# Kernel tuning notes

Hardware: AMD Instinct MI355X
Metric: run time of the kernel (lower is better)

The kernel has to match this reference:

```python
import jax, jax.numpy as jnp
import numpy as np

N = 50000
E = 800000
IN_C = 512
HID = 256
OUT_C = 2
NUM_LAYERS = 3
NUM_HIER = 3
EPS = 1e-5


def setup_inputs() -> dict:
    key = jax.random.key(0)
    ks = jax.random.split(key, 24)
    g = lambda k, shp, fan: jax.random.normal(k, shp, jnp.float32) / np.sqrt(fan)
    inp = {
        "x": jax.random.normal(ks[0], (N, IN_C), jnp.float32),
        "edge_index": jax.random.randint(ks[1], (2, E), 0, N, jnp.int64),
        # GCN conv weights/biases
        "conv_w0": g(ks[2], (IN_C, HID), IN_C),
        "conv_ws": g(ks[3], (NUM_LAYERS - 1, HID, HID), HID),
        "conv_b": jnp.zeros((NUM_LAYERS, HID), jnp.float32),
        "bn_g": jnp.ones((NUM_LAYERS, HID), jnp.float32),
        "bn_b": jnp.zeros((NUM_LAYERS, HID), jnp.float32),
        # global-path MLPs
        "fcg_w0": g(ks[4], (HID, HID), HID),
        "fcg_ws": g(ks[5], (NUM_HIER - 1, 2 * HID, HID), 2 * HID),
        "fcg_b": jnp.zeros((NUM_HIER, HID), jnp.float32),
        "bng_g": jnp.ones((NUM_HIER, HID), jnp.float32),
        "bng_b": jnp.zeros((NUM_HIER, HID), jnp.float32),
        # local-path MLPs
        "fcl_w": g(ks[6], (NUM_HIER, HID, HID), HID),
        "fcl_b": jnp.zeros((NUM_HIER, HID), jnp.float32),
        "bnl_g": jnp.ones((NUM_HIER, HID), jnp.float32),
        "bnl_b": jnp.zeros((NUM_HIER, HID), jnp.float32),
        # output heads
        "outg_w": g(ks[7], (HID, OUT_C), HID),
        "outg_b": jnp.zeros((OUT_C,), jnp.float32),
        "outl_w": g(ks[8], (NUM_HIER, HID, OUT_C), HID),
        "outl_b": jnp.zeros((NUM_HIER, OUT_C), jnp.float32),
    }
    return inp


def _gcn_edges(edge_index):
    # add self-loops, compute symmetric normalization D^-1/2 (A+I) D^-1/2
    loops = jnp.arange(N, dtype=edge_index.dtype)
    rows = jnp.concatenate([edge_index[0], loops])
    cols = jnp.concatenate([edge_index[1], loops])
    deg = jax.ops.segment_sum(jnp.ones_like(rows, jnp.float32), rows, num_segments=N)
    dinv = jnp.where(deg > 0, jax.lax.rsqrt(deg), 0.0)
    w = dinv[rows] * dinv[cols]
    return rows, cols, w


def _propagate(h, rows, cols, w):
    msg = h[cols] * w[:, None]          # [E+N, HID] gather
    return jax.ops.segment_sum(msg, rows, num_segments=N)


def _bn(h, gamma, beta):
    m = h.mean(0)
    v = h.var(0)
    return gamma * (h - m) * jax.lax.rsqrt(v + EPS) + beta


def reference(x, edge_index, conv_w0, conv_ws, conv_b, bn_g, bn_b,
              fcg_w0, fcg_ws, fcg_b, bng_g, bng_b,
              fcl_w, fcl_b, bnl_g, bnl_b,
              outg_w, outg_b, outl_w, outl_b):
    rows, cols, ew = _gcn_edges(edge_index)
    h = x
    for i in range(NUM_LAYERS):
        W = conv_w0 if i == 0 else conv_ws[i - 1]
        h = _propagate(h @ W, rows, cols, ew) + conv_b[i]
        h = jax.nn.relu(_bn(h, bn_g[i], bn_b[i]))  # dropout = identity (eval)
    # hierarchical global path
    hg = []
    xg = jax.nn.relu(_bn(h @ fcg_w0 + fcg_b[0], bng_g[0], bng_b[0]))
    hg.append(xg)
    for i in range(NUM_HIER - 1):
        xg = jnp.concatenate([hg[i], h], -1) @ fcg_ws[i] + fcg_b[i + 1]
        xg = jax.nn.relu(_bn(xg, bng_g[i + 1], bng_b[i + 1]))
        hg.append(xg)
    og = jax.nn.log_softmax(hg[-1] @ outg_w + outg_b, axis=-1)
    # local heads
    ol = []
    for i in range(NUM_HIER):
        hl = jax.nn.relu(_bn(hg[i] @ fcl_w[i] + fcl_b[i], bnl_g[i], bnl_b[i]))
        ol.append(jax.nn.log_softmax(hl @ outl_w[i] + outl_b[i], axis=-1))
    # stack: [1 + NUM_HIER, N, OUT_C] (og first, then local heads)
    return jnp.stack([og] + ol, axis=0)
```

## Files before the change

kernel.cpp:

```cpp
#include <hip/hip_runtime.h>
#include <math.h>

#define N_NODES 50000
#define E_EDGES 800000
#define HID 256
#define EPS_BN 1e-5f

typedef __attribute__((ext_vector_type(8))) short short8;
typedef __attribute__((ext_vector_type(4))) float floatx4;
typedef __attribute__((ext_vector_type(8))) unsigned short ushort8v;

__device__ __forceinline__ unsigned short f2bf(float f) {
    unsigned u = __float_as_uint(f);
    u = (u + 0x7FFFu + ((u >> 16) & 1u)) >> 16;
    return (unsigned short)u;
}
__device__ __forceinline__ float bf2f(unsigned short b) {
    return __uint_as_float(((unsigned)b) << 16);
}
__device__ __forceinline__ void bn_scsh(const float* stats, const float* gamma,
                                        const float* beta, int ch,
                                        float& sc, float& sh) {
    const float invn = 1.0f / (float)N_NODES;
    float mean = stats[ch] * invn;
    float var = stats[HID + ch] * invn - mean * mean;
    var = fmaxf(var, 0.f);
    sc = gamma[ch] * rsqrtf(var + EPS_BN);
    sh = beta[ch] - mean * sc;
}

__global__ __launch_bounds__(256) void k_deg(const int* __restrict__ rows,
                                             int* __restrict__ deg) {
    int e = blockIdx.x * 256 + threadIdx.x;
    atomicAdd(&deg[rows[e]], 1);
}

__global__ __launch_bounds__(256) void k_dinv(const int* __restrict__ deg,
                                              float* __restrict__ dinv) {
    int n = blockIdx.x * 256 + threadIdx.x;
    if (n < N_NODES) dinv[n] = rsqrtf((float)deg[n] + 1.0f);
}

__global__ __launch_bounds__(1024) void k_scan(const int* __restrict__ deg,
                                               int* __restrict__ rowptr) {
    __shared__ int wsum[16];
    __shared__ int carry_s;
    int tid = threadIdx.x, lane = tid & 63, w = tid >> 6;
    if (tid == 0) carry_s = 0;
    __syncthreads();
    for (int base = 0; base < N_NODES; base += 1024) {
        int v = (base + tid < N_NODES) ? deg[base + tid] : 0;
        int x = v;
#pragma unroll
        for (int d = 1; d < 64; d <<= 1) {
            int t = __shfl_up(x, d);
            if (lane >= d) x += t;
        }
        if (lane == 63) wsum[w] = x;
        __syncthreads();
        if (w == 0) {
            int ws = (lane < 16) ? wsum[lane] : 0;
#pragma unroll
            for (int d = 1; d < 16; d <<= 1) {
                int t = __shfl_up(ws, d);
                if (lane >= d) ws += t;
            }
            if (lane < 16) wsum[lane] = ws;
        }
        __syncthreads();
        int c = carry_s;
        int wbase = (w > 0) ? wsum[w - 1] : 0;
        if (base + tid < N_NODES) rowptr[base + tid] = c + wbase + x - v;
        __syncthreads();
        if (tid == 0) carry_s = c + wsum[15];
        __syncthreads();
    }
    if (threadIdx.x == 0) rowptr[N_NODES] = carry_s;
}

__global__ __launch_bounds__(256) void k_fill(const int* __restrict__ rows,
                                              const int* __restrict__ cols,
                                              const int* __restrict__ rowptr,
                                              int* __restrict__ cursor,
                                              int* __restrict__ colidx) {
    int e = blockIdx.x * 256 + threadIdx.x;
    int r = rows[e];
    int pos = atomicAdd(&cursor[r], 1);
    colidx[rowptr[r] + pos] = cols[e];
}

__global__ __launch_bounds__(256) void k_f2bf_vec(const float* __restrict__ X,
                                                  unsigned short* __restrict__ Y,
                                                  int n4) {
    int i = blockIdx.x * 256 + threadIdx.x;
    if (i >= n4) return;
    float4 v = ((const float4*)X)[i];
    ushort4 o;
    o.x = f2bf(v.x); o.y = f2bf(v.y); o.z = f2bf(v.z); o.w = f2bf(v.w);
    ((ushort4*)Y)[i] = o;
}

__global__ __launch_bounds__(256) void k_wt(const float* __restrict__ W,
                                            unsigned short* __restrict__ Wt,
                                            int K) {
    int idx = blockIdx.x * 256 + threadIdx.x;
    if (idx >= K * HID) return;
    int k = idx >> 8;
    int n = idx & (HID - 1);
    Wt[(size_t)n * K + k] = f2bf(W[idx]);
}

__global__ __launch_bounds__(256) void k_gemm_mfma(
    const unsigned short* __restrict__ A0, int lda0,
    const unsigned short* __restrict__ A1, int lda1, int K0, int K,
    const unsigned short* __restrict__ Bt,
    unsigned short* __restrict__ C,
    const float* __restrict__ rowscale,
    float* __restrict__ stats)
{
    __shared__ alignas(16) unsigned short As[128 * 32];
    __shared__ alignas(16) unsigned short Bs[128 * 32];
    int tid = threadIdx.x;
    int wid = tid >> 6, lane = tid & 63;
    int row0 = blockIdx.x * 128;
    int n0 = blockIdx.y * 128;
    int wrow = (wid & 1) * 64, wcol = (wid >> 1) * 64;
    int lr = lane >> 2;
    int lk = (lane & 3) * 8;
    int qq = lane >> 4, mr = lane & 15;

    floatx4 acc[4][4];
#pragma unroll
    for (int i = 0; i < 4; ++i)
#pragma unroll
        for (int j = 0; j < 4; ++j) {
            floatx4 z = {0.f, 0.f, 0.f, 0.f};
            acc[i][j] = z;
        }

    for (int k0 = 0; k0 < K; k0 += 32) {
        const unsigned short* Abase;
        int lda;
        if (k0 < K0) { Abase = A0 + k0; lda = lda0; }
        else         { Abase = A1 + (k0 - K0); lda = lda1; }
#pragma unroll
        for (int i = 0; i < 2; ++i) {
            int rloc = wid * 32 + i * 16 + lr;
            int grow = row0 + rloc;
            if (grow > N_NODES - 1) grow = N_NODES - 1;
            const unsigned short* g = Abase + (size_t)grow * lda + lk;
            unsigned short* l = As + (wid * 32 + i * 16) * 32;
            __builtin_amdgcn_global_load_lds(
                (const __attribute__((address_space(1))) void*)g,
                (__attribute__((address_space(3))) void*)l, 16, 0, 0);
        }
#pragma unroll
        for (int i = 0; i < 2; ++i) {
            int nloc = wid * 32 + i * 16 + lr;
            const unsigned short* g = Bt + (size_t)(n0 + nloc) * K + k0 + lk;
            unsigned short* l = Bs + (wid * 32 + i * 16) * 32;
            __builtin_amdgcn_global_load_lds(
                (const __attribute__((address_space(1))) void*)g,
                (__attribute__((address_space(3))) void*)l, 16, 0, 0);
        }
        __syncthreads();
        short8 af[4], bfv[4];
#pragma unroll
        for (int i = 0; i < 4; ++i)
            af[i] = *(const short8*)(As + (wrow + i * 16 + mr) * 32 + qq * 8);
#pragma unroll
        for (int j = 0; j < 4; ++j)
            bfv[j] = *(const short8*)(Bs + (wcol + j * 16 + mr) * 32 + qq * 8);
#pragma unroll
        for (int i = 0; i < 4; ++i)
#pragma unroll
            for (int j = 0; j < 4; ++j)
                acc[i][j] = __builtin_amdgcn_mfma_f32_16x16x32_bf16(
                    af[i], bfv[j], acc[i][j], 0, 0, 0);
        __syncthreads();
    }

    float* ls = (float*)As;
    float* lq = ((float*)As) + 128;
    if (stats) {
        ((float*)As)[tid] = 0.f;
        __syncthreads();
    }

    float psum[4] = {0.f, 0.f, 0.f, 0.f};
    float psq[4]  = {0.f, 0.f, 0.f, 0.f};
#pragma unroll
    for (int i = 0; i < 4; ++i) {
        int rbase = row0 + wrow + i * 16 + qq * 4;
#pragma unroll
        for (int r = 0; r < 4; ++r) {
            int row = rbase + r;
            if (row >= N_NODES) continue;
            float rs = rowscale ? rowscale[row] : 1.0f;
            unsigned short* cp = C + (size_t)row * HID + n0 + wcol + mr;
#pragma unroll
            for (int j = 0; j < 4; ++j) {
                float v = acc[i][j][r] * rs;
                cp[j * 16] = f2bf(v);
                psum[j] += v;
                psq[j] += v * v;
            }
        }
    }
    if (stats) {
#pragma unroll
        for (int j = 0; j < 4; ++j) {
            int lc = wcol + j * 16 + mr;
            atomicAdd(&ls[lc], psum[j]);
            atomicAdd(&lq[lc], psq[j]);
        }
        __syncthreads();
        if (tid < 128) atomicAdd(&stats[n0 + tid], ls[tid]);
        else atomicAdd(&stats[HID + n0 + (tid - 128)], lq[tid - 128]);
    }
}

__global__ __launch_bounds__(256) void k_aggregate_bf(
    const unsigned short* __restrict__ g,
    unsigned short* __restrict__ outp,
    const int* __restrict__ rowptr,
    const int* __restrict__ colidx,
    const float* __restrict__ dinv,
    float* __restrict__ stats) {
    int lane = threadIdx.x & 63;
    int gw = blockIdx.x * 4 + (threadIdx.x >> 6);
    int totw = gridDim.x * 4;
    float s0 = 0.f, s1 = 0.f, s2 = 0.f, s3 = 0.f;
    float q0 = 0.f, q1 = 0.f, q2 = 0.f, q3 = 0.f;
    for (int node = gw; node < N_NODES; node += totw) {
        int s = rowptr[node], e = rowptr[node + 1];
        ushort4 sv = ((const ushort4*)(g + (size_t)node * HID))[lane];
        float a0 = bf2f(sv.x), a1 = bf2f(sv.y), a2 = bf2f(sv.z), a3 = bf2f(sv.w);
        for (int base = s; base < e; base += 64) {
            int cnt = e - base; if (cnt > 64) cnt = 64;
            int cidx = (lane < cnt) ? colidx[base + lane] : 0;
            int j = 0;
            for (; j + 4 <= cnt; j += 4) {
                int c0 = __shfl(cidx, j + 0), c1 = __shfl(cidx, j + 1);
                int c2 = __shfl(cidx, j + 2), c3 = __shfl(cidx, j + 3);
                ushort4 v0 = ((const ushort4*)(g + (size_t)c0 * HID))[lane];
                ushort4 v1 = ((const ushort4*)(g + (size_t)c1 * HID))[lane];
                ushort4 v2 = ((const ushort4*)(g + (size_t)c2 * HID))[lane];
                ushort4 v3 = ((const ushort4*)(g + (size_t)c3 * HID))[lane];
                a0 += (bf2f(v0.x) + bf2f(v1.x)) + (bf2f(v2.x) + bf2f(v3.x));
                a1 += (bf2f(v0.y) + bf2f(v1.y)) + (bf2f(v2.y) + bf2f(v3.y));
                a2 += (bf2f(v0.z) + bf2f(v1.z)) + (bf2f(v2.z) + bf2f(v3.z));
                a3 += (bf2f(v0.w) + bf2f(v1.w)) + (bf2f(v2.w) + bf2f(v3.w));
            }
            for (; j < cnt; ++j) {
                int c = __shfl(cidx, j);
                ushort4 v = ((const ushort4*)(g + (size_t)c * HID))[lane];
                a0 += bf2f(v.x); a1 += bf2f(v.y); a2 += bf2f(v.z); a3 += bf2f(v.w);
            }
        }
        float rs = dinv[node];
        a0 *= rs; a1 *= rs; a2 *= rs; a3 *= rs;
        ushort4 o;
        o.x = f2bf(a0); o.y = f2bf(a1); o.z = f2bf(a2); o.w = f2bf(a3);
        ((ushort4*)(outp + (size_t)node * HID))[lane] = o;
        s0 += a0; s1 += a1; s2 += a2; s3 += a3;
        q0 += a0 * a0; q1 += a1 * a1; q2 += a2 * a2; q3 += a3 * a3;
    }
    __shared__ float ls[HID], lq[HID];
    ls[threadIdx.x] = 0.f; lq[threadIdx.x] = 0.f;
    __syncthreads();
    atomicAdd(&ls[lane * 4 + 0], s0); atomicAdd(&lq[lane * 4 + 0], q0);
    atomicAdd(&ls[lane * 4 + 1], s1); atomicAdd(&lq[lane * 4 + 1], q1);
    atomicAdd(&ls[lane * 4 + 2], s2); atomicAdd(&lq[lane * 4 + 2], q2);
    atomicAdd(&ls[lane * 4 + 3], s3); atomicAdd(&lq[lane * 4 + 3], q3);
    __syncthreads();
    atomicAdd(&stats[threadIdx.x], ls[threadIdx.x]);
    atomicAdd(&stats[HID + threadIdx.x], lq[threadIdx.x]);
}

__global__ __launch_bounds__(256) void k_bnapply_bf(const unsigned short* __restrict__ X,
                                                    unsigned short* __restrict__ Y,
                                                    const float* __restrict__ stats,
                                                    const float* __restrict__ gamma,
                                                    const float* __restrict__ beta) {
    int i = blockIdx.x * 256 + threadIdx.x;
    int ch8 = (i & 31) * 8;
    ushort8v v = *(const ushort8v*)(X + (size_t)i * 8);
    ushort8v o;
#pragma unroll
    for (int k = 0; k < 8; ++k) {
        float sc, sh;
        bn_scsh(stats, gamma, beta, ch8 + k, sc, sh);
        float f = bf2f((unsigned short)v[k]);
        o[k] = f2bf(fmaxf(f * sc + sh, 0.f));
    }
    *(ushort8v*)(Y + (size_t)i * 8) = o;
}

__global__ __launch_bounds__(256) void k_head_bf(const unsigned short* __restrict__ H,
                                                 const float* __restrict__ stats,
                                                 const float* __restrict__ gamma,
                                                 const float* __restrict__ beta,
                                                 const float* __restrict__ W,
                                                 const float* __restrict__ b,
                                                 float* __restrict__ outp) {
    int wave = (blockIdx.x * 256 + threadIdx.x) >> 6;
    int lane = threadIdx.x & 63;
    if (wave >= N_NODES) return;
    ushort4 h4 = ((const ushort4*)(H + (size_t)wave * HID))[lane];
    float h0 = bf2f(h4.x), h1 = bf2f(h4.y), h2 = bf2f(h4.z), h3 = bf2f(h4.w);
    if (stats) {
        int ch = lane * 4;
        float sc, sh;
        bn_scsh(stats, gamma, beta, ch + 0, sc, sh); h0 = fmaxf(h0 * sc + sh, 0.f);
        bn_scsh(stats, gamma, beta, ch + 1, sc, sh); h1 = fmaxf(h1 * sc + sh, 0.f);
        bn_scsh(stats, gamma, beta, ch + 2, sc, sh); h2 = fmaxf(h2 * sc + sh, 0.f);
        bn_scsh(stats, gamma, beta, ch + 3, sc, sh); h3 = fmaxf(h3 * sc + sh, 0.f);
    }
    const float2* W2 = (const float2*)W;
    float2 w0 = W2[lane * 4 + 0], w1 = W2[lane * 4 + 1];
    float2 w2 = W2[lane * 4 + 2], w3 = W2[lane * 4 + 3];
    float p0 = h0 * w0.x + h1 * w1.x + h2 * w2.x + h3 * w3.x;
    float p1 = h0 * w0.y + h1 * w1.y + h2 * w2.y + h3 * w3.y;
    for (int off = 32; off > 0; off >>= 1) {
        p0 += __shfl_down(p0, off);
        p1 += __shfl_down(p1, off);
    }
    if (lane == 0) {
        float z0 = p0 + b[0], z1 = p1 + b[1];
        float m = fmaxf(z0, z1);
        float lse = m + logf(expf(z0 - m) + expf(z1 - m));
        outp[(size_t)wave * 2 + 0] = z0 - lse;
        outp[(size_t)wave * 2 + 1] = z1 - lse;
    }
}

extern "C" void kernel_launch(void* const* d_in, const int* in_sizes, int n_in,
                              void* d_out, int out_size, void* d_ws, size_t ws_size,
                              hipStream_t stream) {
    const float* x       = (const float*)d_in[0];
    const int*   ei      = (const int*)d_in[1];
    const float* conv_w0 = (const float*)d_in[2];
    const float* conv_ws = (const float*)d_in[3];
    const float* bn_g    = (const float*)d_in[5];
    const float* bn_b    = (const float*)d_in[6];
    const float* fcg_w0  = (const float*)d_in[7];
    const float* fcg_ws  = (const float*)d_in[8];
    const float* bng_g   = (const float*)d_in[10];
    const float* bng_b   = (const float*)d_in[11];
    const float* fcl_w   = (const float*)d_in[12];
    const float* bnl_g   = (const float*)d_in[14];
    const float* bnl_b   = (const float*)d_in[15];
    const float* outg_w  = (const float*)d_in[16];
    const float* outg_b  = (const float*)d_in[17];
    const float* outl_w  = (const float*)d_in[18];
    const float* outl_b  = (const float*)d_in[19];
    float* out = (float*)d_out;

    const int* rows = ei;
    const int* cols = ei + E_EDGES;

    char* ws = (char*)d_ws;
    size_t off = 0;
    auto carve = [&](size_t bytes) -> void* {
        void* p = ws + off;
        off = (off + bytes + 255) & ~(size_t)255;
        return p;
    };
    const size_t ACT = (size_t)N_NODES * HID * 2;
    unsigned short* xbf = (unsigned short*)carve((size_t)N_NODES * 512 * 2);
    unsigned short* tG  = (unsigned short*)carve(ACT);
    unsigned short* tA  = (unsigned short*)carve(ACT);
    unsigned short* hbf = (unsigned short*)carve(ACT);
    unsigned short* g1  = (unsigned short*)carve(ACT);
    unsigned short* g2  = (unsigned short*)carve(ACT);
    unsigned short* wt_conv0 = (unsigned short*)carve(256 * 512 * 2);
    unsigned short* wt_conv1 = (unsigned short*)carve(256 * 256 * 2);
    unsigned short* wt_conv2 = (unsigned short*)carve(256 * 256 * 2);
    unsigned short* wt_fcg0  = (unsigned short*)carve(256 * 256 * 2);
    unsigned short* wt_fcgs0 = (unsigned short*)carve(256 * 512 * 2);
    unsigned short* wt_fcgs1 = (unsigned short*)carve(256 * 512 * 2);
    unsigned short* wt_fcl0  = (unsigned short*)carve(256 * 256 * 2);
    unsigned short* wt_fcl1  = (unsigned short*)carve(256 * 256 * 2);
    unsigned short* wt_fcl2  = (unsigned short*)carve(256 * 256 * 2);
    int*   deg    = (int*)carve(2 * 50048 * 4);
    int*   cursor = deg + 50048;
    int*   rowptr = (int*)carve((size_t)(N_NODES + 1) * 4);
    float* dinv   = (float*)carve((size_t)N_NODES * 4);
    int*   colidx = (int*)carve((size_t)E_EDGES * 4);
    float* stats_all = (float*)carve(9 * 2 * HID * 4);
    (void)off; (void)ws_size; (void)in_sizes; (void)n_in; (void)out_size;

    hipMemsetAsync(deg, 0, 2 * 50048 * 4, stream);
    hipMemsetAsync(stats_all, 0, 9 * 2 * HID * 4, stream);
    k_deg<<<E_EDGES / 256, 256, 0, stream>>>(rows, deg);
    k_dinv<<<(N_NODES + 255) / 256, 256, 0, stream>>>(deg, dinv);
    k_scan<<<1, 1024, 0, stream>>>(deg, rowptr);
    k_fill<<<E_EDGES / 256, 256, 0, stream>>>(rows, cols, rowptr, cursor, colidx);

    k_f2bf_vec<<<(N_NODES * 512 / 4 + 255) / 256, 256, 0, stream>>>(x, xbf, N_NODES * 512 / 4);
    k_wt<<<(512 * 256 + 255) / 256, 256, 0, stream>>>(conv_w0, wt_conv0, 512);
    k_wt<<<(256 * 256 + 255) / 256, 256, 0, stream>>>(conv_ws, wt_conv1, 256);
    k_wt<<<(256 * 256 + 255) / 256, 256, 0, stream>>>(conv_ws + 65536, wt_conv2, 256);
    k_wt<<<(256 * 256 + 255) / 256, 256, 0, stream>>>(fcg_w0, wt_fcg0, 256);
    k_wt<<<(512 * 256 + 255) / 256, 256, 0, stream>>>(fcg_ws, wt_fcgs0, 512);
    k_wt<<<(512 * 256 + 255) / 256, 256, 0, stream>>>(fcg_ws + 131072, wt_fcgs1, 512);
    k_wt<<<(256 * 256 + 255) / 256, 256, 0, stream>>>(fcl_w, wt_fcl0, 256);
    k_wt<<<(256 * 256 + 255) / 256, 256, 0, stream>>>(fcl_w + 65536, wt_fcl1, 256);
    k_wt<<<(256 * 256 + 255) / 256, 256, 0, stream>>>(fcl_w + 131072, wt_fcl2, 256);

    dim3 ggrid((N_NODES + 127) / 128, 2);
    auto gemm = [&](const unsigned short* A0, int lda0,
                    const unsigned short* A1, int lda1, int K0, int K,
                    const unsigned short* Bt, unsigned short* C,
                    const float* rs, float* st) {
        k_gemm_mfma<<<ggrid, 256, 0, stream>>>(A0, lda0, A1, lda1, K0, K, Bt, C, rs, st);
    };
    auto bnapply = [&](float* st, const unsigned short* X, unsigned short* Y,
                       const float* gamma, const float* beta) {
        k_bnapply_bf<<<N_NODES * 32 / 256, 256, 0, stream>>>(X, Y, st, gamma, beta);
    };
    auto agg = [&](const unsigned short* in, unsigned short* outb, float* st) {
        k_aggregate_bf<<<782, 256, 0, stream>>>(in, outb, rowptr, colidx, dinv, st);
    };
    float* st;

    st = stats_all + 0 * 512;
    gemm(xbf, 512, nullptr, 0, 512, 512, wt_conv0, tG, dinv, nullptr);
    agg(tG, tA, st);
    bnapply(st, tA, g1, bn_g + 0, bn_b + 0);
    st = stats_all + 1 * 512;
    gemm(g1, 256, nullptr, 0, 256, 256, wt_conv1, tG, dinv, nullptr);
    agg(tG, tA, st);
    bnapply(st, tA, g2, bn_g + 256, bn_b + 256);
    st = stats_all + 2 * 512;
    gemm(g2, 256, nullptr, 0, 256, 256, wt_conv2, tG, dinv, nullptr);
    agg(tG, tA, st);
    bnapply(st, tA, hbf, bn_g + 512, bn_b + 512);

    st = stats_all + 3 * 512;
    gemm(hbf, 256, nullptr, 0, 256, 256, wt_fcg0, tG, nullptr, st);
    bnapply(st, tG, g1, bng_g + 0, bng_b + 0);
    st = stats_all + 4 * 512;
    gemm(g1, 256, nullptr, 0, 256, 256, wt_fcl0, tG, nullptr, st);
    k_head_bf<<<N_NODES / 4, 256, 0, stream>>>(tG, st, bnl_g + 0, bnl_b + 0,
                                               outl_w, outl_b,
                                               out + (size_t)1 * N_NODES * 2);
    st = stats_all + 5 * 512;
    gemm(g1, 256, hbf, 256, 256, 512, wt_fcgs0, tG, nullptr, st);
    bnapply(st, tG, g2, bng_g + 256, bng_b + 256);
    st = stats_all + 6 * 512;
    gemm(g2, 256, nullptr, 0, 256, 256, wt_fcl1, tG, nullptr, st);
    k_head_bf<<<N_NODES / 4, 256, 0, stream>>>(tG, st, bnl_g + 256, bnl_b + 256,
                                               outl_w + 512, outl_b + 2,
                                               out + (size_t)2 * N_NODES * 2);
    st = stats_all + 7 * 512;
    gemm(g2, 256, hbf, 256, 256, 512, wt_fcgs1, tG, nullptr, st);
    bnapply(st, tG, g1, bng_g + 512, bng_b + 512);
    st = stats_all + 8 * 512;
    gemm(g1, 256, nullptr, 0, 256, 256, wt_fcl2, tG, nullptr, st);
    k_head_bf<<<N_NODES / 4, 256, 0, stream>>>(tG, st, bnl_g + 512, bnl_b + 512,
                                               outl_w + 1024, outl_b + 4,
                                               out + (size_t)3 * N_NODES * 2);
    k_head_bf<<<N_NODES / 4, 256, 0, stream>>>(g1, nullptr, nullptr, nullptr,
                                               outg_w, outg_b, out);
}
```

Measured before the change: 1.070 ms.

## Store activations in 32-channel sliced layout to localize aggregation gathers

```diff
diff --git a/kernel.cpp b/kernel.cpp
--- a/kernel.cpp
+++ b/kernel.cpp
@@ -5,6 +5,8 @@
 #define E_EDGES 800000
 #define HID 256
 #define EPS_BN 1e-5f
+
+#define AGG_BPS 192
 
 typedef __attribute__((ext_vector_type(8))) short short8;
 typedef __attribute__((ext_vector_type(4))) float floatx4;
@@ -89,15 +91,19 @@
     colidx[rowptr[r] + pos] = cols[e];
 }
 
-__global__ __launch_bounds__(256) void k_f2bf_vec(const float* __restrict__ X,
-                                                  unsigned short* __restrict__ Y,
-                                                  int n4) {
+__global__ __launch_bounds__(256) void k_f2bf_slice(const float* __restrict__ X,
+                                                    unsigned short* __restrict__ Y) {
     int i = blockIdx.x * 256 + threadIdx.x;
-    if (i >= n4) return;
-    float4 v = ((const float4*)X)[i];
-    ushort4 o;
-    o.x = f2bf(v.x); o.y = f2bf(v.y); o.z = f2bf(v.z); o.w = f2bf(v.w);
-    ((ushort4*)Y)[i] = o;
+    int slice = i / (N_NODES * 4);
+    int rem = i - slice * (N_NODES * 4);
+    int node = rem >> 2, p8 = rem & 3;
+    const float* xp = X + (size_t)node * 512 + slice * 32 + p8 * 8;
+    float4 va = ((const float4*)xp)[0];
+    float4 vb = ((const float4*)xp)[1];
+    ushort8v o;
+    o[0] = f2bf(va.x); o[1] = f2bf(va.y); o[2] = f2bf(va.z); o[3] = f2bf(va.w);
+    o[4] = f2bf(vb.x); o[5] = f2bf(vb.y); o[6] = f2bf(vb.z); o[7] = f2bf(vb.w);
+    *(ushort8v*)(Y + (size_t)i * 8) = o;
 }
 
 __global__ __launch_bounds__(256) void k_wt(const float* __restrict__ W,
@@ -111,8 +117,8 @@
 }
 
 __global__ __launch_bounds__(256) void k_gemm_mfma(
-    const unsigned short* __restrict__ A0, int lda0,
-    const unsigned short* __restrict__ A1, int lda1, int K0, int K,
+    const unsigned short* __restrict__ A0,
+    const unsigned short* __restrict__ A1, int K0, int K,
     const unsigned short* __restrict__ Bt,
     unsigned short* __restrict__ C,
     const float* __restrict__ rowscale,
@@ -139,16 +145,15 @@
         }
 
     for (int k0 = 0; k0 < K; k0 += 32) {
-        const unsigned short* Abase;
-        int lda;
-        if (k0 < K0) { Abase = A0 + k0; lda = lda0; }
-        else         { Abase = A1 + (k0 - K0); lda = lda1; }
+        const unsigned short* Abase =
+            (k0 < K0) ? A0 + (size_t)(k0 >> 5) * (N_NODES * 32)
+                      : A1 + (size_t)((k0 - K0) >> 5) * (N_NODES * 32);
 #pragma unroll
         for (int i = 0; i < 2; ++i) {
             int rloc = wid * 32 + i * 16 + lr;
             int grow = row0 + rloc;
             if (grow > N_NODES - 1) grow = N_NODES - 1;
-            const unsigned short* g = Abase + (size_t)grow * lda + lk;
+            const unsigned short* g = Abase + (size_t)grow * 32 + lk;
             unsigned short* l = As + (wid * 32 + i * 16) * 32;
             __builtin_amdgcn_global_load_lds(
                 (const __attribute__((address_space(1))) void*)g,
@@ -197,11 +202,11 @@
             int row = rbase + r;
             if (row >= N_NODES) continue;
             float rs = rowscale ? rowscale[row] : 1.0f;
-            unsigned short* cp = C + (size_t)row * HID + n0 + wcol + mr;
 #pragma unroll
             for (int j = 0; j < 4; ++j) {
+                int col = n0 + wcol + j * 16 + mr;
                 float v = acc[i][j][r] * rs;
-                cp[j * 16] = f2bf(v);
+                C[((size_t)(col >> 5) * N_NODES + row) * 32 + (col & 31)] = f2bf(v);
                 psum[j] += v;
                 psq[j] += v * v;
             }
@@ -228,54 +233,77 @@
     const float* __restrict__ dinv,
     float* __restrict__ stats) {
     int lane = threadIdx.x & 63;
-    int gw = blockIdx.x * 4 + (threadIdx.x >> 6);
-    int totw = gridDim.x * 4;
-    float s0 = 0.f, s1 = 0.f, s2 = 0.f, s3 = 0.f;
-    float q0 = 0.f, q1 = 0.f, q2 = 0.f, q3 = 0.f;
-    for (int node = gw; node < N_NODES; node += totw) {
+    int wid = threadIdx.x >> 6;
+    int slice = blockIdx.x & 7;
+    int bslice = blockIdx.x >> 3;
+    const unsigned short* gs = g + (size_t)slice * (N_NODES * 32);
+    unsigned short* os = outp + (size_t)slice * (N_NODES * 32);
+    int g8 = lane >> 3;
+    int l8 = lane & 7;
+    int wv = bslice * 4 + wid;
+    const int nw = AGG_BPS * 4;
+
+    __shared__ float ls[32], lq[32];
+    if (threadIdx.x < 32) { ls[threadIdx.x] = 0.f; lq[threadIdx.x] = 0.f; }
+    __syncthreads();
+
+    float sa0 = 0.f, sa1 = 0.f, sa2 = 0.f, sa3 = 0.f;
+    float qa0 = 0.f, qa1 = 0.f, qa2 = 0.f, qa3 = 0.f;
+
+    for (int node = wv; node < N_NODES; node += nw) {
         int s = rowptr[node], e = rowptr[node + 1];
-        ushort4 sv = ((const ushort4*)(g + (size_t)node * HID))[lane];
-        float a0 = bf2f(sv.x), a1 = bf2f(sv.y), a2 = bf2f(sv.z), a3 = bf2f(sv.w);
-        for (int base = s; base < e; base += 64) {
-            int cnt = e - base; if (cnt > 64) cnt = 64;
-            int cidx = (lane < cnt) ? colidx[base + lane] : 0;
-            int j = 0;
-            for (; j + 4 <= cnt; j += 4) {
-                int c0 = __shfl(cidx, j + 0), c1 = __shfl(cidx, j + 1);
-                int c2 = __shfl(cidx, j + 2), c3 = __shfl(cidx, j + 3);
-                ushort4 v0 = ((const ushort4*)(g + (size_t)c0 * HID))[lane];
-                ushort4 v1 = ((const ushort4*)(g + (size_t)c1 * HID))[lane];
-                ushort4 v2 = ((const ushort4*)(g + (size_t)c2 * HID))[lane];
-                ushort4 v3 = ((const ushort4*)(g + (size_t)c3 * HID))[lane];
-                a0 += (bf2f(v0.x) + bf2f(v1.x)) + (bf2f(v2.x) + bf2f(v3.x));
-                a1 += (bf2f(v0.y) + bf2f(v1.y)) + (bf2f(v2.y) + bf2f(v3.y));
-                a2 += (bf2f(v0.z) + bf2f(v1.z)) + (bf2f(v2.z) + bf2f(v3.z));
-                a3 += (bf2f(v0.w) + bf2f(v1.w)) + (bf2f(v2.w) + bf2f(v3.w));
-            }
-            for (; j < cnt; ++j) {
-                int c = __shfl(cidx, j);
-                ushort4 v = ((const ushort4*)(g + (size_t)c * HID))[lane];
-                a0 += bf2f(v.x); a1 += bf2f(v.y); a2 += bf2f(v.z); a3 += bf2f(v.w);
-            }
-        }
-        float rs = dinv[node];
-        a0 *= rs; a1 *= rs; a2 *= rs; a3 *= rs;
-        ushort4 o;
-        o.x = f2bf(a0); o.y = f2bf(a1); o.z = f2bf(a2); o.w = f2bf(a3);
-        ((ushort4*)(outp + (size_t)node * HID))[lane] = o;
-        s0 += a0; s1 += a1; s2 += a2; s3 += a3;
-        q0 += a0 * a0; q1 += a1 * a1; q2 += a2 * a2; q3 += a3 * a3;
-    }
-    __shared__ float ls[HID], lq[HID];
-    ls[threadIdx.x] = 0.f; lq[threadIdx.x] = 0.f;
+        float a0 = 0.f, a1 = 0.f, a2 = 0.f, a3 = 0.f;
+        for (int base = s; base < e; base += 16) {
+            int e1 = e - 1;
+            int i0 = base + g8, i1 = base + 8 + g8;
+            int j0 = i0 < e1 ? i0 : e1;
+            int j1 = i1 < e1 ? i1 : e1;
+            int c0 = __builtin_nontemporal_load(&colidx[j0]);
+            int c1 = __builtin_nontemporal_load(&colidx[j1]);
+            float m0 = (i0 < e) ? 1.f : 0.f;
+            float m1 = (i1 < e) ? 1.f : 0.f;
+            ushort4 v0 = *(const ushort4*)(gs + (c0 << 5) + (l8 << 2));
+            ushort4 v1 = *(const ushort4*)(gs + (c1 << 5) + (l8 << 2));
+            a0 = fmaf(m0, bf2f(v0.x), a0); a1 = fmaf(m0, bf2f(v0.y), a1);
+            a2 = fmaf(m0, bf2f(v0.z), a2); a3 = fmaf(m0, bf2f(v0.w), a3);
+            a0 = fmaf(m1, bf2f(v1.x), a0); a1 = fmaf(m1, bf2f(v1.y), a1);
+            a2 = fmaf(m1, bf2f(v1.z), a2); a3 = fmaf(m1, bf2f(v1.w), a3);
+        }
+#pragma unroll
+        for (int off = 8; off < 64; off <<= 1) {
+            a0 += __shfl_xor(a0, off);
+            a1 += __shfl_xor(a1, off);
+            a2 += __shfl_xor(a2, off);
+            a3 += __shfl_xor(a3, off);
+        }
+        if (lane < 8) {
+            ushort4 sv = *(const ushort4*)(gs + (node << 5) + (l8 << 2));
+            float rs = dinv[node];
+            float r0 = (a0 + bf2f(sv.x)) * rs;
+            float r1 = (a1 + bf2f(sv.y)) * rs;
+            float r2 = (a2 + bf2f(sv.z)) * rs;
+            float r3 = (a3 + bf2f(sv.w)) * rs;
+            ushort4 o;
+            o.x = f2bf(r0); o.y = f2bf(r1); o.z = f2bf(r2); o.w = f2bf(r3);
+            union { ushort4 u4; unsigned long long u64; } cvt;
+            cvt.u4 = o;
+            __builtin_nontemporal_store(
+                cvt.u64, (unsigned long long*)(os + (node << 5) + (l8 << 2)));
+            sa0 += r0; sa1 += r1; sa2 += r2; sa3 += r3;
+            qa0 += r0 * r0; qa1 += r1 * r1; qa2 += r2 * r2; qa3 += r3 * r3;
+        }
+    }
+    if (lane < 8) {
+        atomicAdd(&ls[l8 * 4 + 0], sa0); atomicAdd(&lq[l8 * 4 + 0], qa0);
+        atomicAdd(&ls[l8 * 4 + 1], sa1); atomicAdd(&lq[l8 * 4 + 1], qa1);
+        atomicAdd(&ls[l8 * 4 + 2], sa2); atomicAdd(&lq[l8 * 4 + 2], qa2);
+        atomicAdd(&ls[l8 * 4 + 3], sa3); atomicAdd(&lq[l8 * 4 + 3], qa3);
+    }
     __syncthreads();
-    atomicAdd(&ls[lane * 4 + 0], s0); atomicAdd(&lq[lane * 4 + 0], q0);
-    atomicAdd(&ls[lane * 4 + 1], s1); atomicAdd(&lq[lane * 4 + 1], q1);
-    atomicAdd(&ls[lane * 4 + 2], s2); atomicAdd(&lq[lane * 4 + 2], q2);
-    atomicAdd(&ls[lane * 4 + 3], s3); atomicAdd(&lq[lane * 4 + 3], q3);
-    __syncthreads();
-    atomicAdd(&stats[threadIdx.x], ls[threadIdx.x]);
-    atomicAdd(&stats[HID + threadIdx.x], lq[threadIdx.x]);
+    if (threadIdx.x < 32) {
+        atomicAdd(&stats[slice * 32 + threadIdx.x], ls[threadIdx.x]);
+        atomicAdd(&stats[HID + slice * 32 + threadIdx.x], lq[threadIdx.x]);
+    }
 }
 
 __global__ __launch_bounds__(256) void k_bnapply_bf(const unsigned short* __restrict__ X,
@@ -284,7 +312,9 @@
                                                     const float* __restrict__ gamma,
                                                     const float* __restrict__ beta) {
     int i = blockIdx.x * 256 + threadIdx.x;
-    int ch8 = (i & 31) * 8;
+    int slice = i / (N_NODES * 4);
+    int rem = i - slice * (N_NODES * 4);
+    int ch8 = slice * 32 + (rem & 3) * 8;
     ushort8v v = *(const ushort8v*)(X + (size_t)i * 8);
     ushort8v o;
 #pragma unroll
@@ -307,7 +337,8 @@
     int wave = (blockIdx.x * 256 + threadIdx.x) >> 6;
     int lane = threadIdx.x & 63;
     if (wave >= N_NODES) return;
-    ushort4 h4 = ((const ushort4*)(H + (size_t)wave * HID))[lane];
+    ushort4 h4 = *(const ushort4*)(
+        H + ((size_t)(lane >> 3) * N_NODES + wave) * 32 + (lane & 7) * 4);
     float h0 = bf2f(h4.x), h1 = bf2f(h4.y), h2 = bf2f(h4.z), h3 = bf2f(h4.w);
     if (stats) {
         int ch = lane * 4;
@@ -398,7 +429,7 @@
     k_scan<<<1, 1024, 0, stream>>>(deg, rowptr);
     k_fill<<<E_EDGES / 256, 256, 0, stream>>>(rows, cols, rowptr, cursor, colidx);
 
-    k_f2bf_vec<<<(N_NODES * 512 / 4 + 255) / 256, 256, 0, stream>>>(x, xbf, N_NODES * 512 / 4);
+    k_f2bf_slice<<<N_NODES * 64 / 256, 256, 0, stream>>>(x, xbf);
     k_wt<<<(512 * 256 + 255) / 256, 256, 0, stream>>>(conv_w0, wt_conv0, 512);
     k_wt<<<(256 * 256 + 255) / 256, 256, 0, stream>>>(conv_ws, wt_conv1, 256);
     k_wt<<<(256 * 256 + 255) / 256, 256, 0, stream>>>(conv_ws + 65536, wt_conv2, 256);
@@ -410,55 +441,55 @@
     k_wt<<<(256 * 256 + 255) / 256, 256, 0, stream>>>(fcl_w + 131072, wt_fcl2, 256);
 
     dim3 ggrid((N_NODES + 127) / 128, 2);
-    auto gemm = [&](const unsigned short* A0, int lda0,
-                    const unsigned short* A1, int lda1, int K0, int K,
-                    const unsigned short* Bt, unsigned short* C,
+    auto gemm = [&](const unsigned short* A0, const unsigned short* A1,
+                    int K0, int K, const unsigned short* Bt, unsigned short* C,
                     const float* rs, float* st) {
-        k_gemm_mfma<<<ggrid, 256, 0, stream>>>(A0, lda0, A1, lda1, K0, K, Bt, C, rs, st);
+        k_gemm_mfma<<<ggrid, 256, 0, stream>>>(A0, A1, K0, K, Bt, C, rs, st);
     };
     auto bnapply = [&](float* st, const unsigned short* X, unsigned short* Y,
                        const float* gamma, const float* beta) {
         k_bnapply_bf<<<N_NODES * 32 / 256, 256, 0, stream>>>(X, Y, st, gamma, beta);
     };
     auto agg = [&](const unsigned short* in, unsigned short* outb, float* st) {
-        k_aggregate_bf<<<782, 256, 0, stream>>>(in, outb, rowptr, colidx, dinv, st);
+        k_aggregate_bf<<<8 * AGG_BPS, 256, 0, stream>>>(in, outb, rowptr, colidx,
+                                                        dinv, st);
     };
     float* st;
 
     st = stats_all + 0 * 512;
-    gemm(xbf, 512, nullptr, 0, 512, 512, wt_conv0, tG, dinv, nullptr);
+    gemm(xbf, nullptr, 512, 512, wt_conv0, tG, dinv, nullptr);
     agg(tG, tA, st);
     bnapply(st, tA, g1, bn_g + 0, bn_b + 0);
     st = stats_all + 1 * 512;
-    gemm(g1, 256, nullptr, 0, 256, 256, wt_conv1, tG, dinv, nullptr);
+    gemm(g1, nullptr, 256, 256, wt_conv1, tG, dinv, nullptr);
     agg(tG, tA, st);
     bnapply(st, tA, g2, bn_g + 256, bn_b + 256);
     st = stats_all + 2 * 512;
-    gemm(g2, 256, nullptr, 0, 256, 256, wt_conv2, tG, dinv, nullptr);
+    gemm(g2, nullptr, 256, 256, wt_conv2, tG, dinv, nullptr);
     agg(tG, tA, st);
     bnapply(st, tA, hbf, bn_g + 512, bn_b + 512);
 
     st = stats_all + 3 * 512;
-    gemm(hbf, 256, nullptr, 0, 256, 256, wt_fcg0, tG, nullptr, st);
+    gemm(hbf, nullptr, 256, 256, wt_fcg0, tG, nullptr, st);
     bnapply(st, tG, g1, bng_g + 0, bng_b + 0);
     st = stats_all + 4 * 512;
-    gemm(g1, 256, nullptr, 0, 256, 256, wt_fcl0, tG, nullptr, st);
+    gemm(g1, nullptr, 256, 256, wt_fcl0, tG, nullptr, st);
     k_head_bf<<<N_NODES / 4, 256, 0, stream>>>(tG, st, bnl_g + 0, bnl_b + 0,
                                                outl_w, outl_b,
                                                out + (size_t)1 * N_NODES * 2);
     st = stats_all + 5 * 512;
-    gemm(g1, 256, hbf, 256, 256, 512, wt_fcgs0, tG, nullptr, st);
+    gemm(g1, hbf, 256, 512, wt_fcgs0, tG, nullptr, st);
     bnapply(st, tG, g2, bng_g + 256, bng_b + 256);
     st = stats_all + 6 * 512;
-    gemm(g2, 256, nullptr, 0, 256, 256, wt_fcl1, tG, nullptr, st);
+    gemm(g2, nullptr, 256, 256, wt_fcl1, tG, nullptr, st);
     k_head_bf<<<N_NODES / 4, 256, 0, stream>>>(tG, st, bnl_g + 256, bnl_b + 256,
                                                outl_w + 512, outl_b + 2,
                                                out + (size_t)2 * N_NODES * 2);
     st = stats_all + 7 * 512;
-    gemm(g2, 256, hbf, 256, 256, 512, wt_fcgs1, tG, nullptr, st);
+    gemm(g2, hbf, 256, 512, wt_fcgs1, tG, nullptr, st);
     bnapply(st, tG, g1, bng_g + 512, bng_b + 512);
     st = stats_all + 8 * 512;
-    gemm(g1, 256, nullptr, 0, 256, 256, wt_fcl2, tG, nullptr, st);
+    gemm(g1, nullptr, 256, 256, wt_fcl2, tG, nullptr, st);
     k_head_bf<<<N_NODES / 4, 256, 0, stream>>>(tG, st, bnl_g + 512, bnl_b + 512,
                                                outl_w + 1024, outl_b + 4,
                                                out + (size_t)3 * N_NODES * 2);
```

Measured after the change: 1.319 ms. 23.3% more time.
